# Performance work log

Measured on AMD Instinct MI355X. Metric: run time of the kernel, lower is better.

The kernel has to match this reference:

```python
import jax, jax.numpy as jnp
import numpy as np

INPUT_SIZE = 2048
HIDDEN_SIZE = 4096
NUM_CLASSES = 1000
BATCH = 4096


def setup_inputs() -> dict:
    key = jax.random.key(0)
    kx, k1, k2, k3 = jax.random.split(key, 4)
    x = jax.random.normal(kx, (BATCH, INPUT_SIZE), dtype=jnp.float32)
    w1 = jax.random.normal(k1, (INPUT_SIZE, HIDDEN_SIZE), dtype=jnp.float32) * 0.01
    b1 = jnp.zeros((HIDDEN_SIZE,), dtype=jnp.float32)
    w2 = jax.random.normal(k2, (HIDDEN_SIZE, HIDDEN_SIZE), dtype=jnp.float32) * 0.01
    b2 = jnp.zeros((HIDDEN_SIZE,), dtype=jnp.float32)
    w3 = jax.random.normal(k3, (HIDDEN_SIZE, NUM_CLASSES), dtype=jnp.float32) * 0.01
    b3 = jnp.zeros((NUM_CLASSES,), dtype=jnp.float32)
    return {"x": x, "w1": w1, "b1": b1, "w2": w2, "b2": b2, "w3": w3, "b3": b3}


def reference(x, w1, b1, w2, b2, w3, b3):
    # fused GEMM + bias + ReLU, equivalent to the original Python double-loop matmul
    h1 = jax.nn.relu(x @ w1 + b1)    # [B, H]
    h2 = jax.nn.relu(h1 @ w2 + b2)   # [B, H]
    out = h2 @ w3 + b3               # [B, C]
    return out
```

## Files before the change

kernel.cpp:

```cpp
#include <hip/hip_runtime.h>
#include <hip/hip_bf16.h>

typedef __bf16 bf16x8 __attribute__((ext_vector_type(8)));
typedef __bf16 bf16x4 __attribute__((ext_vector_type(4)));
typedef float floatx4 __attribute__((ext_vector_type(4)));

#define B_    4096
#define IN_   2048
#define HID_  4096
#define NC_   1000
#define NCP_  1024

__device__ __forceinline__ void transpose_cvt_dev(const float* __restrict__ src,
                                                  __bf16* __restrict__ dst,
                                                  int R, int C, int bx, int by,
                                                  float* tile ) {
    const int r0 = bx * 64;
    const int c0 = by * 64;
    const int t  = threadIdx.x;
#pragma unroll
    for (int it = 0; it < 4; ++it) {
        int lin = it * 256 + t;
        int sr = lin >> 4, c4 = lin & 15;
        int cb = c0 + c4 * 4;
        const float* s = src + (size_t)(r0 + sr) * C;
        float4 v;
        if (cb + 3 < C) {
            v = *(const float4*)(s + cb);
        } else {
            v.x = (cb + 0 < C) ? s[cb + 0] : 0.f;
            v.y = (cb + 1 < C) ? s[cb + 1] : 0.f;
            v.z = (cb + 2 < C) ? s[cb + 2] : 0.f;
            v.w = (cb + 3 < C) ? s[cb + 3] : 0.f;
        }
        tile[(c4 * 4 + 0) * 65 + sr] = v.x;
        tile[(c4 * 4 + 1) * 65 + sr] = v.y;
        tile[(c4 * 4 + 2) * 65 + sr] = v.z;
        tile[(c4 * 4 + 3) * 65 + sr] = v.w;
    }
    __syncthreads();
#pragma unroll
    for (int it = 0; it < 2; ++it) {
        int lin = it * 256 + t;
        int dr = lin >> 3, q8 = lin & 7;
        bf16x8 o;
#pragma unroll
        for (int j = 0; j < 8; ++j) o[j] = (__bf16)tile[dr * 65 + q8 * 8 + j];
        *(bf16x8*)(dst + (size_t)(c0 + dr) * R + r0 + q8 * 8) = o;
    }
}

__device__ __forceinline__ void swizzle32x32(int bid, int& bx, int& by) {
    int xcd = bid & 7;
    int q   = bid >> 3;
    by = ((xcd >> 2) << 4) + (q & 15);
    bx = ((xcd & 3) << 3) + (q >> 4);
}

template <bool RELU, bool OUT_BF16>
__device__ __forceinline__ void gemm_core(const __bf16* __restrict__ A,
                                          const __bf16* __restrict__ Bt,
                                          const float* __restrict__ bias,
                                          void* __restrict__ Cv,
                                          int M, int K, int Nstore,
                                          int bx, int by,
                                          __bf16* sA, __bf16* sB) {
    const int tid   = threadIdx.x;
    const int lane  = tid & 63;
    const int wave  = tid >> 6;
    const int wr    = wave >> 1;
    const int wc    = wave & 1;
    const int mBase = by * 128;
    const int nBase = bx * 128;
    const int lr    = lane >> 4;
    const int lc    = lane & 15;

    floatx4 acc[4][4];
#pragma unroll
    for (int i = 0; i < 4; ++i)
#pragma unroll
        for (int j = 0; j < 4; ++j) acc[i][j] = (floatx4)0.f;

    for (int k0 = 0; k0 < K; k0 += 64) {
#pragma unroll
        for (int it = 0; it < 4; ++it) {
            int lin = it * 256 + tid;
            int r   = lin >> 3;
            int kc  = (lin & 7) ^ (r & 7);
            const __bf16* ga = A  + (size_t)(mBase + r) * K + k0 + kc * 8;
            const __bf16* gb = Bt + (size_t)(nBase + r) * K + k0 + kc * 8;
            __builtin_amdgcn_global_load_lds(
                (__attribute__((address_space(1))) void*)ga,
                (__attribute__((address_space(3))) void*)(sA + lin * 8), 16, 0, 0);
            __builtin_amdgcn_global_load_lds(
                (__attribute__((address_space(1))) void*)gb,
                (__attribute__((address_space(3))) void*)(sB + lin * 8), 16, 0, 0);
        }
        __builtin_amdgcn_s_waitcnt(0);
        __syncthreads();

#pragma unroll
        for (int kk = 0; kk < 2; ++kk) {
            const int sw = (kk * 4 + lr) ^ (lc & 7);
            bf16x8 af[4], bfr[4];
#pragma unroll
            for (int i = 0; i < 4; ++i)
                af[i] = *(const bf16x8*)(sA + (wr * 64 + i * 16 + lc) * 64 + sw * 8);
#pragma unroll
            for (int j = 0; j < 4; ++j)
                bfr[j] = *(const bf16x8*)(sB + (wc * 64 + j * 16 + lc) * 64 + sw * 8);
#pragma unroll
            for (int i = 0; i < 4; ++i)
#pragma unroll
                for (int j = 0; j < 4; ++j)
                    acc[i][j] = __builtin_amdgcn_mfma_f32_16x16x32_bf16(af[i], bfr[j], acc[i][j], 0, 0, 0);
        }
        __syncthreads();
    }

#pragma unroll
    for (int j = 0; j < 4; ++j) {
        int col = nBase + wc * 64 + j * 16 + lc;
        if (col < Nstore) {
            float bv = bias[col];
#pragma unroll
            for (int i = 0; i < 4; ++i) {
                int rowb = mBase + wr * 64 + i * 16 + lr * 4;
#pragma unroll
                for (int r = 0; r < 4; ++r) {
                    float v = acc[i][j][r] + bv;
                    if (RELU) v = fmaxf(v, 0.f);
                    if (OUT_BF16)
                        ((__bf16*)Cv)[(size_t)(rowb + r) * Nstore + col] = (__bf16)v;
                    else
                        ((float*)Cv)[(size_t)(rowb + r) * Nstore + col] = v;
                }
            }
        }
    }
}

__global__ __launch_bounds__(256) void prep1(const float* __restrict__ x,
                                             __bf16* __restrict__ xb,
                                             const float* __restrict__ w1,
                                             __bf16* __restrict__ w1t) {
    __shared__ float tile[64 * 65];
    const int b = blockIdx.x;
    if (b < 4096) {
        int i = (b * 256 + (int)threadIdx.x) * 8;
        float4 a = *(const float4*)(x + i);
        float4 c = *(const float4*)(x + i + 4);
        bf16x8 o;
        o[0] = (__bf16)a.x; o[1] = (__bf16)a.y; o[2] = (__bf16)a.z; o[3] = (__bf16)a.w;
        o[4] = (__bf16)c.x; o[5] = (__bf16)c.y; o[6] = (__bf16)c.z; o[7] = (__bf16)c.w;
        *(bf16x8*)(xb + i) = o;
    } else {
        int l = b - 4096;
        transpose_cvt_dev(w1, w1t, IN_, HID_, l & 31, l >> 5, tile);
    }
}

__global__ __launch_bounds__(256, 2) void gemm1_fused(const __bf16* __restrict__ xb,
                                                      const __bf16* __restrict__ w1t,
                                                      const float* __restrict__ b1,
                                                      __bf16* __restrict__ h1,
                                                      const float* __restrict__ w2,
                                                      __bf16* __restrict__ w2t,
                                                      const float* __restrict__ w3,
                                                      __bf16* __restrict__ w3t) {
    __shared__ float smem[8192];
    const int b = blockIdx.x;
    if (b < 1024) {
        __bf16* sA = (__bf16*)smem;
        __bf16* sB = sA + 128 * 64;
        int bx, by;
        swizzle32x32(b, bx, by);
        gemm_core<true, true>(xb, w1t, b1, h1, B_, IN_, HID_, bx, by, sA, sB);
    } else if (b < 5120) {
        int l = b - 1024;
        transpose_cvt_dev(w2, w2t, HID_, HID_, l & 63, l >> 6, smem);
    } else {
        int l = b - 5120;
        transpose_cvt_dev(w3, w3t, HID_, NC_, l & 63, l >> 6, smem);
    }
}

template <bool RELU, bool OUT_BF16>
__global__ __launch_bounds__(256, 2) void gemm_bt(const __bf16* __restrict__ A,
                                                  const __bf16* __restrict__ Bt,
                                                  const float* __restrict__ bias,
                                                  void* __restrict__ Cv,
                                                  int M, int K, int Nstore) {
    __shared__ __bf16 sA[128 * 64];
    __shared__ __bf16 sB[128 * 64];
    int bx = blockIdx.x, by = blockIdx.y;
    if (gridDim.x == 32 && gridDim.y == 32) {
        int bid = by * 32 + bx;
        swizzle32x32(bid, bx, by);
    }
    gemm_core<RELU, OUT_BF16>(A, Bt, bias, Cv, M, K, Nstore, bx, by, sA, sB);
}

__global__ __launch_bounds__(256, 2) void gemm_sk(const __bf16* __restrict__ A,
                                                  const __bf16* __restrict__ Bt,
                                                  float* __restrict__ P,
                                                  int M, int KH, int Ktot) {
    __shared__ __bf16 sA[128 * 64];
    __shared__ __bf16 sB[128 * 64];

    const int tid   = threadIdx.x;
    const int lane  = tid & 63;
    const int wave  = tid >> 6;
    const int wr    = wave >> 1;
    const int wc    = wave & 1;
    const int mBase = blockIdx.y * 128;
    const int nBase = blockIdx.x * 128;
    const int z     = blockIdx.z;
    const int kOff  = z * KH;
    const int lr    = lane >> 4;
    const int lc    = lane & 15;

    floatx4 acc[4][4];
#pragma unroll
    for (int i = 0; i < 4; ++i)
#pragma unroll
        for (int j = 0; j < 4; ++j) acc[i][j] = (floatx4)0.f;

    for (int k0 = kOff; k0 < kOff + KH; k0 += 64) {
#pragma unroll
        for (int it = 0; it < 4; ++it) {
            int lin = it * 256 + tid;
            int r   = lin >> 3;
            int kc  = (lin & 7) ^ (r & 7);
            const __bf16* ga = A  + (size_t)(mBase + r) * Ktot + k0 + kc * 8;
            const __bf16* gb = Bt + (size_t)(nBase + r) * Ktot + k0 + kc * 8;
            __builtin_amdgcn_global_load_lds(
                (__attribute__((address_space(1))) void*)ga,
                (__attribute__((address_space(3))) void*)(sA + lin * 8), 16, 0, 0);
            __builtin_amdgcn_global_load_lds(
                (__attribute__((address_space(1))) void*)gb,
                (__attribute__((address_space(3))) void*)(sB + lin * 8), 16, 0, 0);
        }
        __builtin_amdgcn_s_waitcnt(0);
        __syncthreads();

#pragma unroll
        for (int kk = 0; kk < 2; ++kk) {
            const int sw = (kk * 4 + lr) ^ (lc & 7);
            bf16x8 af[4], bfr[4];
#pragma unroll
            for (int i = 0; i < 4; ++i)
                af[i] = *(const bf16x8*)(sA + (wr * 64 + i * 16 + lc) * 64 + sw * 8);
#pragma unroll
            for (int j = 0; j < 4; ++j)
                bfr[j] = *(const bf16x8*)(sB + (wc * 64 + j * 16 + lc) * 64 + sw * 8);
#pragma unroll
            for (int i = 0; i < 4; ++i)
#pragma unroll
                for (int j = 0; j < 4; ++j)
                    acc[i][j] = __builtin_amdgcn_mfma_f32_16x16x32_bf16(af[i], bfr[j], acc[i][j], 0, 0, 0);
        }
        __syncthreads();
    }

    float* Pz = P + (size_t)z * M * NCP_;
#pragma unroll
    for (int j = 0; j < 4; ++j) {
        int col = nBase + wc * 64 + j * 16 + lc;
#pragma unroll
        for (int i = 0; i < 4; ++i) {
            int rowb = mBase + wr * 64 + i * 16 + lr * 4;
#pragma unroll
            for (int r = 0; r < 4; ++r)
                Pz[(size_t)(rowb + r) * NCP_ + col] = acc[i][j][r];
        }
    }
}

__global__ __launch_bounds__(256) void reduce_bias(const float* __restrict__ P,
                                                   const float* __restrict__ b3,
                                                   float* __restrict__ out) {
    int c = blockIdx.x * 256 + threadIdx.x;
    int m = blockIdx.y;
    if (c < NC_)
        out[(size_t)m * NC_ + c] =
            P[(size_t)m * NCP_ + c] + P[(size_t)(B_ + m) * NCP_ + c] + b3[c];
}

extern "C" void kernel_launch(void* const* d_in, const int* in_sizes, int n_in,
                              void* d_out, int out_size, void* d_ws, size_t ws_size,
                              hipStream_t stream) {
    const float* x  = (const float*)d_in[0];
    const float* w1 = (const float*)d_in[1];
    const float* b1 = (const float*)d_in[2];
    const float* w2 = (const float*)d_in[3];
    const float* b2 = (const float*)d_in[4];
    const float* w3 = (const float*)d_in[5];
    const float* b3 = (const float*)d_in[6];
    float* out = (float*)d_out;

    char* ws = (char*)d_ws;
    __bf16* xb  = (__bf16*)(ws);
    __bf16* w1t = (__bf16*)(ws + (16u << 20));
    __bf16* w2t = (__bf16*)(ws + (32u << 20));
    __bf16* w3t = (__bf16*)(ws + (64u << 20));
    __bf16* h1  = (__bf16*)(ws + (72u << 20));
    __bf16* h2  = (__bf16*)(ws);
    float*  P   = (float*)(ws + (72u << 20));

    prep1<<<6144, 256, 0, stream>>>(x, xb, w1, w1t);

    gemm1_fused<<<6144, 256, 0, stream>>>(xb, w1t, b1, h1, w2, w2t, w3, w3t);

    gemm_bt<true, true><<<dim3(HID_ / 128, B_ / 128), 256, 0, stream>>>(
        h1, w2t, b2, h2, B_, HID_, HID_);

    gemm_sk<<<dim3(NCP_ / 128, B_ / 128, 2), 256, 0, stream>>>(
        h2, w3t, P, B_, HID_ / 2, HID_);
    reduce_bias<<<dim3(NCP_ / 256, B_), 256, 0, stream>>>(P, b3, out);
}
```

Measured before the change: 443.3 us.

## Replace layer-2 GEMM with 256x256-tile, 8-wave, double-buffered direct-to-LDS kernel

The second hidden-layer GEMM (4096x4096x4096) moves from a 128x128-tile kernel to a 256x256-tile kernel with 512 threads and 128KB of dynamic LDS. Operands are double-buffered via global_load_lds with a swizzled layout. Loads are interleaved with quarter-tile MFMA phases under barriers and s_setprio, and blocks are remapped across XCDs for L2 locality. This aims to raise arithmetic intensity and overlap memory with compute. The cost is higher register and LDS pressure, likely limiting occupancy to one block per CU.

```diff
diff --git a/kernel.cpp b/kernel.cpp
--- a/kernel.cpp
+++ b/kernel.cpp
@@ -185,20 +185,136 @@
     }
 }
 
-template <bool RELU, bool OUT_BF16>
-__global__ __launch_bounds__(256, 2) void gemm_bt(const __bf16* __restrict__ A,
-                                                  const __bf16* __restrict__ Bt,
-                                                  const float* __restrict__ bias,
-                                                  void* __restrict__ Cv,
-                                                  int M, int K, int Nstore) {
-    __shared__ __bf16 sA[128 * 64];
-    __shared__ __bf16 sB[128 * 64];
-    int bx = blockIdx.x, by = blockIdx.y;
-    if (gridDim.x == 32 && gridDim.y == 32) {
-        int bid = by * 32 + bx;
-        swizzle32x32(bid, bx, by);
-    }
-    gemm_core<RELU, OUT_BF16>(A, Bt, bias, Cv, M, K, Nstore, bx, by, sA, sB);
+#define QPHASE(pA, pB, qm, qn, ...)                                            \
+  {                                                                            \
+    bf16x8 af0[4], af1[4], bq0[2], bq1[2];                                     \
+    _Pragma("unroll") for (int i_ = 0; i_ < 4; ++i_) {                         \
+      const __bf16* ap_ = (pA) + ((wr * 128 + (qm) * 64 + i_ * 16 + lc) * 64); \
+      af0[i_] = *(const bf16x8*)(ap_ + ((0 + lr) ^ (lc & 7)) * 8);             \
+      af1[i_] = *(const bf16x8*)(ap_ + ((4 + lr) ^ (lc & 7)) * 8);             \
+    }                                                                          \
+    _Pragma("unroll") for (int j_ = 0; j_ < 2; ++j_) {                         \
+      const __bf16* bp_ = (pB) + ((wc * 64 + (qn) * 32 + j_ * 16 + lc) * 64);  \
+      bq0[j_] = *(const bf16x8*)(bp_ + ((0 + lr) ^ (lc & 7)) * 8);             \
+      bq1[j_] = *(const bf16x8*)(bp_ + ((4 + lr) ^ (lc & 7)) * 8);             \
+    }                                                                          \
+    __VA_ARGS__;                                                               \
+    __builtin_amdgcn_s_barrier();                                              \
+    asm volatile("s_waitcnt lgkmcnt(0)" ::: "memory");                         \
+    __builtin_amdgcn_sched_barrier(0);                                         \
+    __builtin_amdgcn_s_setprio(1);                                             \
+    _Pragma("unroll") for (int i_ = 0; i_ < 4; ++i_)                           \
+      _Pragma("unroll") for (int j_ = 0; j_ < 2; ++j_) {                       \
+        acc[(qm) * 4 + i_][(qn) * 2 + j_] =                                    \
+            __builtin_amdgcn_mfma_f32_16x16x32_bf16(                           \
+                af0[i_], bq0[j_], acc[(qm) * 4 + i_][(qn) * 2 + j_], 0, 0, 0); \
+        acc[(qm) * 4 + i_][(qn) * 2 + j_] =                                    \
+            __builtin_amdgcn_mfma_f32_16x16x32_bf16(                           \
+                af1[i_], bq1[j_], acc[(qm) * 4 + i_][(qn) * 2 + j_], 0, 0, 0); \
+      }                                                                        \
+    __builtin_amdgcn_s_setprio(0);                                             \
+    __builtin_amdgcn_s_barrier();                                              \
+  }
+
+__global__ __launch_bounds__(512, 2) void gemm2_256(const __bf16* __restrict__ A,
+                                                    const __bf16* __restrict__ Bt,
+                                                    const float* __restrict__ bias,
+                                                    __bf16* __restrict__ C) {
+    extern __shared__ __bf16 lds[];
+    const int K  = HID_;
+    const int NT = K / 64;
+
+    const int tid  = threadIdx.x;
+    const int lane = tid & 63;
+    const int wave = tid >> 6;
+    const int wr   = wave >> 2;
+    const int wc   = wave & 3;
+    const int lr   = lane >> 4;
+    const int lc   = lane & 15;
+
+    int bid = blockIdx.y * 16 + blockIdx.x;
+    int xcd = bid & 7, q = bid >> 3;
+    const int by = (xcd & 3) * 4 + (q & 3);
+    const int bx = (xcd >> 2) * 8 + (q >> 2);
+    const int mBase = by * 256;
+    const int nBase = bx * 256;
+
+    __bf16* A0buf = lds;
+    __bf16* B0buf = lds + 16384;
+    __bf16* A1buf = lds + 32768;
+    __bf16* B1buf = lds + 49152;
+
+    auto stage_half = [&](const __bf16* __restrict__ src, int rowBase, int k0,
+                          __bf16* dst) {
+#pragma unroll
+        for (int it = 0; it < 2; ++it) {
+            int lin = it * 512 + tid;
+            int rl  = lin >> 3;
+            int kc  = (lin & 7) ^ (rl & 7);
+            const __bf16* gp = src + (size_t)(rowBase + rl) * HID_ + k0 + kc * 8;
+            __builtin_amdgcn_global_load_lds(
+                (__attribute__((address_space(1))) void*)gp,
+                (__attribute__((address_space(3))) void*)(dst + lin * 8), 16, 0, 0);
+        }
+    };
+
+    floatx4 acc[8][4];
+#pragma unroll
+    for (int i = 0; i < 8; ++i)
+#pragma unroll
+        for (int j = 0; j < 4; ++j) acc[i][j] = (floatx4)0.f;
+
+    stage_half(A,  mBase,       0,  A0buf);
+    stage_half(A,  mBase + 128, 0,  A0buf + 8192);
+    stage_half(Bt, nBase,       0,  B0buf);
+    stage_half(Bt, nBase + 128, 0,  B0buf + 8192);
+    stage_half(A,  mBase,       64, A1buf);
+    stage_half(A,  mBase + 128, 64, A1buf + 8192);
+    asm volatile("s_waitcnt vmcnt(4)" ::: "memory");
+    __builtin_amdgcn_s_barrier();
+
+    for (int t = 0; t < NT; t += 2) {
+        QPHASE(A0buf, B0buf, 0, 0, stage_half(Bt, nBase,       (t + 1) * 64, B1buf));
+        QPHASE(A0buf, B0buf, 0, 1, stage_half(Bt, nBase + 128, (t + 1) * 64, B1buf + 8192));
+        QPHASE(A0buf, B0buf, 1, 0, );
+        QPHASE(A0buf, B0buf, 1, 1, );
+        if (t + 2 < NT) {
+            stage_half(A, mBase,       (t + 2) * 64, A0buf);
+            stage_half(A, mBase + 128, (t + 2) * 64, A0buf + 8192);
+            asm volatile("s_waitcnt vmcnt(4)" ::: "memory");
+        } else {
+            asm volatile("s_waitcnt vmcnt(0)" ::: "memory");
+        }
+        __builtin_amdgcn_s_barrier();
+
+        QPHASE(A1buf, B1buf, 0, 0, if (t + 2 < NT) stage_half(Bt, nBase,       (t + 2) * 64, B0buf));
+        QPHASE(A1buf, B1buf, 0, 1, if (t + 2 < NT) stage_half(Bt, nBase + 128, (t + 2) * 64, B0buf + 8192));
+        QPHASE(A1buf, B1buf, 1, 0, );
+        QPHASE(A1buf, B1buf, 1, 1, );
+        if (t + 3 < NT) {
+            stage_half(A, mBase,       (t + 3) * 64, A1buf);
+            stage_half(A, mBase + 128, (t + 3) * 64, A1buf + 8192);
+            asm volatile("s_waitcnt vmcnt(4)" ::: "memory");
+        } else {
+            asm volatile("s_waitcnt vmcnt(0)" ::: "memory");
+        }
+        __builtin_amdgcn_s_barrier();
+    }
+
+#pragma unroll
+    for (int n = 0; n < 4; ++n) {
+        int col = nBase + wc * 64 + n * 16 + lc;
+        float bv = bias[col];
+#pragma unroll
+        for (int m = 0; m < 8; ++m) {
+            int rowb = mBase + wr * 128 + m * 16 + lr * 4;
+#pragma unroll
+            for (int r = 0; r < 4; ++r) {
+                float v = fmaxf(acc[m][n][r] + bv, 0.f);
+                C[(size_t)(rowb + r) * HID_ + col] = (__bf16)v;
+            }
+        }
+    }
 }
 
 __global__ __launch_bounds__(256, 2) void gemm_sk(const __bf16* __restrict__ A,
@@ -308,12 +424,19 @@
     __bf16* h2  = (__bf16*)(ws);
     float*  P   = (float*)(ws + (72u << 20));
 
+    static int attr_done = 0;
+    if (!attr_done) {
+        (void)hipFuncSetAttribute((const void*)gemm2_256,
+                                  hipFuncAttributeMaxDynamicSharedMemorySize,
+                                  131072);
+        attr_done = 1;
+    }
+
     prep1<<<6144, 256, 0, stream>>>(x, xb, w1, w1t);
 
     gemm1_fused<<<6144, 256, 0, stream>>>(xb, w1t, b1, h1, w2, w2t, w3, w3t);
 
-    gemm_bt<true, true><<<dim3(HID_ / 128, B_ / 128), 256, 0, stream>>>(
-        h1, w2t, b2, h2, B_, HID_, HID_);
+    gemm2_256<<<dim3(16, 16), 512, 131072, stream>>>(h1, w2t, b2, h2);
 
     gemm_sk<<<dim3(NCP_ / 128, B_ / 128, 2), 256, 0, stream>>>(
         h2, w3t, P, B_, HID_ / 2, HID_);
```

Result: slower. 453.6 us (+2.3%).
